# Performance work log

Hardware: AMD Instinct MI355X
Metric: run time of the kernel (lower is better)

## Reference

```python
import jax, jax.numpy as jnp
import numpy as np

B_J0 = 0.01
BETA = 1.8
GAMMA = 0.5
LENS = 0.5
HIGHT = 0.15
SCALE = 6.0
H1, H2, D_IN, D_OUT = 256, 256, 700, 20
BATCH, T = 128, 250


def spike_fn(x):
    # forward of ActFun_adp: Heaviside
    return (x > 0).astype(x.dtype)


def mem_update_adp(inputs, mem, spike, tau_adp, b, tau_m):
    alpha = jnp.exp(-1.0 / tau_m)
    ro = jnp.exp(-1.0 / tau_adp)
    b = ro * b + (1.0 - ro) * spike
    B = B_J0 + BETA * b
    mem = mem * alpha + (1.0 - alpha) * inputs - B * spike
    spike = spike_fn(mem - B)
    return mem, spike, b


def setup_inputs() -> dict:
    key = jax.random.key(0)
    ks = jax.random.split(key, 16)
    inp = {
        "x": jax.random.uniform(ks[0], (BATCH, T, D_IN), jnp.float32),
        "mem1_0": jax.random.uniform(ks[1], (BATCH, H1), jnp.float32),
        "mem2_0": jax.random.uniform(ks[2], (BATCH, H2), jnp.float32),
        "memo_0": jax.random.uniform(ks[3], (BATCH, D_OUT), jnp.float32),
        "Wi1": jax.random.normal(ks[4], (H1, D_IN), jnp.float32) * 0.05,
        "bi1": jnp.zeros((H1,), jnp.float32),
        "W11": jax.random.normal(ks[5], (H1, H1), jnp.float32) * 0.05,
        "b11": jnp.zeros((H1,), jnp.float32),
        "W12": jax.random.normal(ks[6], (H2, H1), jnp.float32) * 0.05,
        "b12": jnp.zeros((H2,), jnp.float32),
        "W22": jax.random.normal(ks[7], (H2, H2), jnp.float32) * 0.05,
        "b22": jnp.zeros((H2,), jnp.float32),
        "Wo": jax.random.normal(ks[8], (D_OUT, H2), jnp.float32) * 0.05,
        "bo": jnp.zeros((D_OUT,), jnp.float32),
        "tau_adp_h1": 150.0 + 10.0 * jax.random.normal(ks[9], (H1,), jnp.float32),
        "tau_adp_h2": 150.0 + 10.0 * jax.random.normal(ks[10], (H2,), jnp.float32),
        "tau_m_h1": 20.0 + 5.0 * jax.random.normal(ks[11], (H1,), jnp.float32),
        "tau_m_h2": 20.0 + 5.0 * jax.random.normal(ks[12], (H2,), jnp.float32),
        "tau_m_o": 20.0 + 5.0 * jax.random.normal(ks[13], (D_OUT,), jnp.float32),
    }
    return inp


def reference(x, mem1_0, mem2_0, memo_0, Wi1, bi1, W11, b11, W12, b12,
              W22, b22, Wo, bo, tau_adp_h1, tau_adp_h2, tau_m_h1, tau_m_h2, tau_m_o):
    B = x.shape[0]
    sp1_0 = jnp.zeros_like(mem1_0)
    sp2_0 = jnp.zeros_like(mem2_0)
    b1_0 = jnp.full_like(mem1_0, B_J0)
    b2_0 = jnp.full_like(mem2_0, B_J0)
    acc0 = jnp.zeros((B, Wo.shape[0]), x.dtype)
    alpha_o = jnp.exp(-1.0 / tau_m_o)

    def step(carry, inp):
        x_t, i = inp
        mem1, sp1, b1, mem2, sp2, b2, memo, acc = carry
        h1_in = x_t @ Wi1.T + bi1 + sp1 @ W11.T + b11
        mem1, sp1, b1 = mem_update_adp(h1_in, mem1, sp1, tau_adp_h1, b1, tau_m_h1)
        h2_in = sp1 @ W12.T + b12 + sp2 @ W22.T + b22
        mem2, sp2, b2 = mem_update_adp(h2_in, mem2, sp2, tau_adp_h2, b2, tau_m_h2)
        memo = memo * alpha_o + (1.0 - alpha_o) * (sp2 @ Wo.T + bo)
        acc = acc + jnp.where(i > 10, jax.nn.softmax(memo, axis=1), 0.0)
        return (mem1, sp1, b1, mem2, sp2, b2, memo, acc), None

    xs = jnp.swapaxes(x, 0, 1)  # [T, B, D_in]
    ts = jnp.arange(xs.shape[0])
    carry, _ = jax.lax.scan(step, (mem1_0, sp1_0, b1_0, mem2_0, sp2_0, b2_0, memo_0, acc0), (xs, ts))
    return carry[-1]  # accumulated softmax output [B, D_out]
```

## Files before the change

### kernel.cpp

```cpp
#include <hip/hip_runtime.h>
#include <math.h>

#define BATCH 128
#define T 250
#define D_IN 700
#define H 256
#define D_OUT 20

typedef float v2f __attribute__((ext_vector_type(2)));
typedef __attribute__((ext_vector_type(8))) short bf16x8;
typedef __attribute__((ext_vector_type(4))) float f32x4;
typedef __attribute__((ext_vector_type(4))) unsigned u32x4;

static __device__ __forceinline__ unsigned short f2b(float f) {
    unsigned u = __float_as_uint(f);
    u += 0x7FFFu + ((u >> 16) & 1u);
    return (unsigned short)(u >> 16);
}

static __device__ __forceinline__ void bar() {
    asm volatile("s_waitcnt lgkmcnt(0)" ::: "memory");
    __builtin_amdgcn_s_barrier();
    asm volatile("" ::: "memory");
}

#define PIDX(c) (10 * ((c) >> 3) + ((c) & 7))
#define QIDX(c) (6 * ((c) >> 2) + ((c) & 3))

#define N_C1 (257 * 512)
#define N_C2 (257 * 288)
#define N_WP (256 * 704)

__global__ void prep_k(const float* __restrict__ Wi1, const float* __restrict__ W11,
                       const float* __restrict__ W12, const float* __restrict__ W22,
                       const float* __restrict__ Wo,
                       unsigned short* __restrict__ Wi1p, unsigned short* __restrict__ C1,
                       unsigned short* __restrict__ C2) {
    int idx = blockIdx.x * 256 + threadIdx.x;
    if (idx < N_C1) {
        int k = idx >> 9, p = idx & 511;
        float v = 0.f;
        if (k < H) v = (p < 256) ? W12[p * H + k] : W11[(p - 256) * H + k];
        C1[idx] = f2b(v);
        return;
    }
    idx -= N_C1;
    if (idx < N_C2) {
        int k = idx / 288, p = idx - k * 288;
        float v = 0.f;
        if (k < H) {
            if (p < 256) v = W22[p * H + k];
            else if (p - 256 < D_OUT) v = Wo[(p - 256) * H + k];
        }
        C2[idx] = f2b(v);
        return;
    }
    idx -= N_C2;
    if (idx < N_WP) {
        int h = idx / 704, k = idx - h * 704;
        Wi1p[idx] = (k < D_IN) ? f2b(Wi1[h * D_IN + k]) : (unsigned short)0;
    }
}

__global__ __launch_bounds__(256) void gemm_u_k(const float* __restrict__ x,
                                                const unsigned short* __restrict__ Wi1p,
                                                const float* __restrict__ bi1,
                                                float* __restrict__ U) {
    const int lane = threadIdx.x & 63;
    const int wv = threadIdx.x >> 6;
    const int quad = lane >> 4;
    const int nl = lane & 15;
    const int mbase = blockIdx.x * 64 + wv * 16;
    const int m = mbase + nl;

    f32x4 acc[16];
#pragma unroll
    for (int i = 0; i < 16; ++i) acc[i] = (f32x4)(0.f);

    float bias[16];
#pragma unroll
    for (int nt = 0; nt < 16; ++nt) bias[nt] = bi1[nt * 16 + nl];

    const float* xrow = x + (size_t)m * D_IN;
    const unsigned short* brow = Wi1p + nl * 704 + quad * 8;

    for (int k0 = 0; k0 < 704; k0 += 32) {
        int ka = k0 + quad * 8;
        int ka2 = (ka + 4 <= 696) ? ka + 4 : 696;
        float4 q0 = *(const float4*)(xrow + ka);
        float4 q1 = *(const float4*)(xrow + ka2);
        bf16x8 af;
        af[0] = (short)f2b(q0.x); af[1] = (short)f2b(q0.y);
        af[2] = (short)f2b(q0.z); af[3] = (short)f2b(q0.w);
        af[4] = (short)f2b(q1.x); af[5] = (short)f2b(q1.y);
        af[6] = (short)f2b(q1.z); af[7] = (short)f2b(q1.w);

        const unsigned short* bp = brow + k0;
        bf16x8 bf[16];
#pragma unroll
        for (int nt = 0; nt < 16; ++nt)
            bf[nt] = *(const bf16x8*)(bp + nt * 16 * 704);
#pragma unroll
        for (int nt = 0; nt < 16; ++nt)
            acc[nt] = __builtin_amdgcn_mfma_f32_16x16x32_bf16(af, bf[nt], acc[nt], 0, 0, 0);
    }

#pragma unroll
    for (int nt = 0; nt < 16; ++nt) {
#pragma unroll
        for (int r = 0; r < 4; ++r) {
            U[(size_t)(mbase + quad * 4 + r) * H + nt * 16 + nl] = acc[nt][r] + bias[nt];
        }
    }
}

static __device__ __forceinline__ void ld8b(const unsigned* __restrict__ L, int c,
                                            const unsigned short* __restrict__ Cb,
                                            unsigned l8, u32x4* b) {
    uint4 ia = *(const uint4*)(L + c);
    uint4 ib = *(const uint4*)(L + c + 4);
    unsigned I[8] = {ia.x, ia.y, ia.z, ia.w, ib.x, ib.y, ib.z, ib.w};
#pragma unroll
    for (int jj = 0; jj < 8; ++jj)
        b[jj] = *(const u32x4*)(Cb + ((unsigned)I[jj] << 9) + l8);
}

static __device__ __forceinline__ void acc8b(const u32x4* b, v2f* a) {
#pragma unroll
    for (int jj = 0; jj < 8; ++jj) {
#pragma unroll
        for (int q = 0; q < 4; ++q) {
            unsigned u = b[jj][q];
            v2f t;
            t.x = __uint_as_float(u << 16);
            t.y = __uint_as_float(u & 0xffff0000u);
            a[q] += t;
        }
    }
}

static __device__ __forceinline__ void gatherB(const unsigned* __restrict__ L, int n,
                                               const unsigned short* __restrict__ Cb,
                                               unsigned l8, v2f* a) {
    a[0] = (v2f)(0.f); a[1] = (v2f)(0.f); a[2] = (v2f)(0.f); a[3] = (v2f)(0.f);
    int nr = (n + 7) & ~7;
    if (nr == 0) return;
    u32x4 x[8], y[8];
    ld8b(L, 0, Cb, l8, x);
    if (nr == 8) { acc8b(x, a); return; }
    ld8b(L, 8, Cb, l8, y);
    int c = 16;
    for (; c + 16 <= nr; c += 16) {
        acc8b(x, a); ld8b(L, c, Cb, l8, x);
        acc8b(y, a); ld8b(L, c + 8, Cb, l8, y);
    }
    if (nr - c == 8) {
        acc8b(x, a); ld8b(L, c, Cb, l8, x);
        acc8b(y, a); acc8b(x, a);
    } else {
        acc8b(x, a); acc8b(y, a);
    }
}

static __device__ __forceinline__ void ld8c(const unsigned* __restrict__ L, int c,
                                            const unsigned short* Cb,
                                            unsigned mo, unsigned ao,
                                            uint2* m, unsigned* av) {
    uint4 ia = *(const uint4*)(L + c);
    uint4 ib = *(const uint4*)(L + c + 4);
    unsigned I[8] = {ia.x, ia.y, ia.z, ia.w, ib.x, ib.y, ib.z, ib.w};
#pragma unroll
    for (int jj = 0; jj < 8; ++jj) {
        const unsigned short* p = Cb + (unsigned)I[jj] * 288u;
        m[jj] = *(const uint2*)(p + mo);
        av[jj] = *(const unsigned*)(p + ao);
    }
}

static __device__ __forceinline__ void acc8c(const uint2* m, const unsigned* av,
                                             v2f* g, v2f& aA) {
#pragma unroll
    for (int jj = 0; jj < 8; ++jj) {
        unsigned u0 = m[jj].x, u1 = m[jj].y, uA = av[jj];
        v2f t0, t1, tA;
        t0.x = __uint_as_float(u0 << 16); t0.y = __uint_as_float(u0 & 0xffff0000u);
        t1.x = __uint_as_float(u1 << 16); t1.y = __uint_as_float(u1 & 0xffff0000u);
        tA.x = __uint_as_float(uA << 16); tA.y = __uint_as_float(uA & 0xffff0000u);
        g[0] += t0; g[1] += t1; aA += tA;
    }
}

static __device__ __forceinline__ void gather2(const unsigned* __restrict__ L, int n,
                                               const unsigned short* Cb,
                                               unsigned mo, unsigned ao,
                                               v2f* g, v2f& aA) {
    g[0] = (v2f)(0.f); g[1] = (v2f)(0.f); aA = (v2f)(0.f);
    int nr = (n + 7) & ~7;
    if (nr == 0) return;
    uint2 xm[8], ym[8]; unsigned xa[8], ya[8];
    ld8c(L, 0, Cb, mo, ao, xm, xa);
    if (nr == 8) { acc8c(xm, xa, g, aA); return; }
    ld8c(L, 8, Cb, mo, ao, ym, ya);
    int c = 16;
    for (; c + 16 <= nr; c += 16) {
        acc8c(xm, xa, g, aA); ld8c(L, c, Cb, mo, ao, xm, xa);
        acc8c(ym, ya, g, aA); ld8c(L, c + 8, Cb, mo, ao, ym, ya);
    }
    if (nr - c == 8) {
        acc8c(xm, xa, g, aA); ld8c(L, c, Cb, mo, ao, xm, xa);
        acc8c(ym, ya, g, aA); acc8c(xm, xa, g, aA);
    } else {
        acc8c(xm, xa, g, aA); acc8c(ym, ya, g, aA);
    }
}

__global__ __launch_bounds__(512, 1) void recurrent_k(
    const float* __restrict__ U,
    const float* __restrict__ mem1_0, const float* __restrict__ mem2_0,
    const float* __restrict__ memo_0,
    const float* __restrict__ b11v, const float* __restrict__ b12v,
    const float* __restrict__ b22v, const float* __restrict__ bov,
    const float* __restrict__ tau_adp_h1, const float* __restrict__ tau_adp_h2,
    const float* __restrict__ tau_m_h1, const float* __restrict__ tau_m_h2,
    const float* __restrict__ tau_m_o,
    const unsigned short* __restrict__ C1b, const unsigned short* __restrict__ C2b,
    float* __restrict__ out)
{
    const int tid = threadIdx.x;
    const int lane = tid & 63;
    const int w = tid >> 6;
    const bool trackA = (w < 4);
    const int wt = w & 3;
    const int bi = blockIdx.x;
    const int j = wt * 64 + lane;
    const unsigned l8 = (unsigned)lane * 8;
    const unsigned mo = (unsigned)lane * 4;
    const unsigned ao = 256u + 2u * (unsigned)(lane & 15);

    __shared__ float PA[4][2][640];
    __shared__ float PB[4][2][432];
    __shared__ __align__(16) unsigned short C2L[193 * 288];
    __shared__ __align__(16) unsigned lists[8][128];

    {
        unsigned* dst = (unsigned*)C2L;
        const unsigned* src = (const unsigned*)C2b;
        for (int i = tid; i < 193 * 144; i += 512)
            dst[i] = (i < 192 * 144) ? src[i] : 0u;
    }
    for (int i = tid; i < 4 * 2 * 640; i += 512) ((float*)PA)[i] = 0.f;
    for (int i = tid; i < 4 * 2 * 432; i += 512) ((float*)PB)[i] = 0.f;

    float mem1 = 0.f, b1 = 0.01f, spk1 = 0.f;
    float al1 = 0.f, ro1 = 0.f, oma1 = 0.f, omr1 = 0.f, b11p = 0.f;
    if (trackA) {
        mem1 = mem1_0[bi * H + j];
        al1 = __expf(-1.f / tau_m_h1[j]);
        ro1 = __expf(-1.f / tau_adp_h1[j]);
        oma1 = 1.f - al1; omr1 = 1.f - ro1;
        b11p = b11v[j];
    }

    float mem2 = 0.f, b2 = 0.01f, spk2 = 0.f;
    float al2 = 0.f, ro2 = 0.f, oma2 = 0.f, omr2 = 0.f, bs2 = 0.f;
    if (!trackA) {
        mem2 = mem2_0[bi * H + j];
        al2 = __expf(-1.f / tau_m_h2[j]);
        ro2 = __expf(-1.f / tau_adp_h2[j]);
        oma2 = 1.f - al2; omr2 = 1.f - ro2;
        bs2 = b12v[j] + b22v[j];
    }

    float memo = 0.f, alo = 0.f, omo = 0.f, bop = 0.f, acco = 0.f;
    const bool outl = (w == 4 && lane < D_OUT);
    if (outl) {
        memo = memo_0[bi * D_OUT + lane];
        alo = __expf(-1.f / tau_m_o[lane]);
        omo = 1.f - alo;
        bop = bov[lane];
    }

    const float* Up = U + (size_t)bi * T * H + j;
    float u_cur = trackA ? *Up : 0.f;
    float u_nxt = 0.f;
    const unsigned long long below = (1ull << lane) - 1ull;

    const int pidx_self = 320 + PIDX(j);
    const int pidx_j = PIDX(j);
    const int qidx_j = QIDX(j);
    const int qidx_out = 384 + 6 * (lane >> 2) + (lane & 3);

    __syncthreads();

    for (int t = 0; t < 252; ++t) {
        const int rbA = (t + 1) & 1;
        const int wbA = t & 1;
        const int rsB = (t + 1) & 1;
        const int wsB = t & 1;

        if (trackA && t < 250) {
            float g11 = PA[0][rbA][pidx_self] + PA[1][rbA][pidx_self] +
                        PA[2][rbA][pidx_self] + PA[3][rbA][pidx_self];
            float h1 = u_cur + b11p + g11;
            b1 = ro1 * b1 + omr1 * spk1;
            float B1 = 0.01f + 1.8f * b1;
            mem1 = mem1 * al1 + oma1 * h1 - B1 * spk1;
            spk1 = (mem1 - B1 > 0.f) ? 1.f : 0.f;

            unsigned long long m = __ballot(spk1 != 0.f);
            int n = __popcll(m);
            unsigned* L = lists[w];
            if (spk1 != 0.f) L[__popcll(m & below)] = (unsigned)j;
            L[n + lane] = 256u;
            asm volatile("s_waitcnt lgkmcnt(0)" ::: "memory");
            __builtin_amdgcn_wave_barrier();

            u_nxt = Up[H];
            Up += H;

            v2f a[4];
            gatherB(L, n, C1b, l8, a);

            float* pw = &PA[wt][wbA][10 * lane];
            *(v2f*)(pw + 0) = a[0];
            *(v2f*)(pw + 2) = a[1];
            *(v2f*)(pw + 4) = a[2];
            *(v2f*)(pw + 6) = a[3];
            u_cur = u_nxt;
        }

        if (w == 4 && t >= 2) {
            float e = 0.f;
            if (lane < D_OUT) {
                float aO = PB[0][rsB][qidx_out] + PB[1][rsB][qidx_out] +
                           PB[2][rsB][qidx_out] + PB[3][rsB][qidx_out];
                memo = memo * alo + omo * (bop + aO);
                e = __expf(memo);
            }
            if (t >= 13) {
                float s = e;
#pragma unroll
                for (int dd = 16; dd >= 1; dd >>= 1) s += __shfl_xor(s, dd, 32);
                if (lane < D_OUT) acco += __fdividef(e, s);
            }
        }

        if (!trackA && t >= 1 && t < 251) {
            float g12 = PA[0][rbA][pidx_j] + PA[1][rbA][pidx_j] +
                        PA[2][rbA][pidx_j] + PA[3][rbA][pidx_j];
            float g22 = PB[0][rsB][qidx_j] + PB[1][rsB][qidx_j] +
                        PB[2][rsB][qidx_j] + PB[3][rsB][qidx_j];
            float h2 = bs2 + g22 + g12;
            b2 = ro2 * b2 + omr2 * spk2;
            float B2 = 0.01f + 1.8f * b2;
            mem2 = mem2 * al2 + oma2 * h2 - B2 * spk2;
            spk2 = (mem2 - B2 > 0.f) ? 1.f : 0.f;

            unsigned long long m = __ballot(spk2 != 0.f);
            int n = __popcll(m);
            unsigned* L = lists[w];
            if (spk2 != 0.f) L[__popcll(m & below)] = (unsigned)j;
            L[n + lane] = (wt == 3) ? 256u : 192u;
            asm volatile("s_waitcnt lgkmcnt(0)" ::: "memory");
            __builtin_amdgcn_wave_barrier();

            v2f g[2]; v2f aA;
            if (wt == 3) {
                gather2(L, n, C2b, mo, ao, g, aA);
            } else {
                gather2(L, n, (const unsigned short*)C2L, mo, ao, g, aA);
            }

            float* pw = &PB[wt][wsB][6 * lane];
            *(v2f*)(pw + 0) = g[0];
            *(v2f*)(pw + 2) = g[1];
            if (lane < 16) {
                float* pa = &PB[wt][wsB][384 + 6 * (lane >> 1) + 2 * (lane & 1)];
                *(v2f*)pa = aA;
            }
        }

        bar();
    }

    if (outl) out[bi * D_OUT + lane] = acco;
}

extern "C" void kernel_launch(void* const* d_in, const int* in_sizes, int n_in,
                              void* d_out, int out_size, void* d_ws, size_t ws_size,
                              hipStream_t stream) {
    const float* x          = (const float*)d_in[0];
    const float* mem1_0     = (const float*)d_in[1];
    const float* mem2_0     = (const float*)d_in[2];
    const float* memo_0     = (const float*)d_in[3];
    const float* Wi1        = (const float*)d_in[4];
    const float* bi1        = (const float*)d_in[5];
    const float* W11        = (const float*)d_in[6];
    const float* b11        = (const float*)d_in[7];
    const float* W12        = (const float*)d_in[8];
    const float* b12        = (const float*)d_in[9];
    const float* W22        = (const float*)d_in[10];
    const float* b22        = (const float*)d_in[11];
    const float* Wo         = (const float*)d_in[12];
    const float* bo         = (const float*)d_in[13];
    const float* tau_adp_h1 = (const float*)d_in[14];
    const float* tau_adp_h2 = (const float*)d_in[15];
    const float* tau_m_h1   = (const float*)d_in[16];
    const float* tau_m_h2   = (const float*)d_in[17];
    const float* tau_m_o    = (const float*)d_in[18];

    float* U = (float*)d_ws;
    unsigned short* C1b  = (unsigned short*)(U + ((size_t)BATCH * T + 1) * H);
    unsigned short* C2b  = C1b + N_C1;
    unsigned short* Wi1p = C2b + N_C2;

    int prep_total = N_C1 + N_C2 + N_WP;
    prep_k<<<(prep_total + 255) / 256, 256, 0, stream>>>(
        Wi1, W11, W12, W22, Wo, Wi1p, C1b, C2b);

    gemm_u_k<<<(BATCH * T) / 64, 256, 0, stream>>>(x, Wi1p, bi1, U);

    recurrent_k<<<BATCH, 512, 0, stream>>>(U, mem1_0, mem2_0, memo_0,
                                           b11, b12, b22, bo,
                                           tau_adp_h1, tau_adp_h2,
                                           tau_m_h1, tau_m_h2, tau_m_o,
                                           C1b, C2b, (float*)d_out);
}
```

Before: 393.3 us.

## Split recurrent layers into paired producer/consumer blocks with global ring handoff

The single 512-thread block per batch row, which ran both layers in lockstep, is split into two 256-thread blocks. One runs layer 1 and publishes its layer-2 input contributions through a 16-slot global ring buffer with progress counters. The layer-2/output block spins on those counters, so the two layers run as a decoupled pipeline with backpressure instead of sharing a per-step barrier. The input projection U is also stored as bf16 to halve its traffic. The cost is spin-wait polling and a reliance on co-residency of paired blocks (256 blocks on the device) to avoid deadlock, plus some bf16 rounding of the input currents.

```diff
diff --git a/kernel.cpp b/kernel.cpp
--- a/kernel.cpp
+++ b/kernel.cpp
@@ -6,6 +6,7 @@
 #define D_IN 700
 #define H 256
 #define D_OUT 20
+#define RING 16
 
 typedef float v2f __attribute__((ext_vector_type(2)));
 typedef __attribute__((ext_vector_type(8))) short bf16x8;
@@ -16,12 +17,6 @@
     unsigned u = __float_as_uint(f);
     u += 0x7FFFu + ((u >> 16) & 1u);
     return (unsigned short)(u >> 16);
-}
-
-static __device__ __forceinline__ void bar() {
-    asm volatile("s_waitcnt lgkmcnt(0)" ::: "memory");
-    __builtin_amdgcn_s_barrier();
-    asm volatile("" ::: "memory");
 }
 
 #define PIDX(c) (10 * ((c) >> 3) + ((c) & 7))
@@ -65,7 +60,7 @@
 __global__ __launch_bounds__(256) void gemm_u_k(const float* __restrict__ x,
                                                 const unsigned short* __restrict__ Wi1p,
                                                 const float* __restrict__ bi1,
-                                                float* __restrict__ U) {
+                                                unsigned short* __restrict__ Ub) {
     const int lane = threadIdx.x & 63;
     const int wv = threadIdx.x >> 6;
     const int quad = lane >> 4;
@@ -109,7 +104,8 @@
     for (int nt = 0; nt < 16; ++nt) {
 #pragma unroll
         for (int r = 0; r < 4; ++r) {
-            U[(size_t)(mbase + quad * 4 + r) * H + nt * 16 + nl] = acc[nt][r] + bias[nt];
+            Ub[(size_t)(mbase + quad * 4 + r) * H + nt * 16 + nl] =
+                f2b(acc[nt][r] + bias[nt]);
         }
     }
 }
@@ -214,8 +210,8 @@
     }
 }
 
-__global__ __launch_bounds__(512, 1) void recurrent_k(
-    const float* __restrict__ U,
+__global__ __launch_bounds__(256, 1) void recurrent_k(
+    const unsigned short* __restrict__ Ub,
     const float* __restrict__ mem1_0, const float* __restrict__ mem2_0,
     const float* __restrict__ memo_0,
     const float* __restrict__ b11v, const float* __restrict__ b12v,
@@ -224,55 +220,122 @@
     const float* __restrict__ tau_m_h1, const float* __restrict__ tau_m_h2,
     const float* __restrict__ tau_m_o,
     const unsigned short* __restrict__ C1b, const unsigned short* __restrict__ C2b,
+    float* __restrict__ G12all, int* __restrict__ prog, int* __restrict__ bdone,
     float* __restrict__ out)
 {
     const int tid = threadIdx.x;
     const int lane = tid & 63;
-    const int w = tid >> 6;
-    const bool trackA = (w < 4);
-    const int wt = w & 3;
-    const int bi = blockIdx.x;
-    const int j = wt * 64 + lane;
-    const unsigned l8 = (unsigned)lane * 8;
-    const unsigned mo = (unsigned)lane * 4;
-    const unsigned ao = 256u + 2u * (unsigned)(lane & 15);
+    const int wt = tid >> 6;
+    const int bi = blockIdx.x >> 1;
+    const bool isA = (blockIdx.x & 1) == 0;
+    const int j = (wt << 6) + lane;
 
     __shared__ float PA[4][2][640];
     __shared__ float PB[4][2][432];
     __shared__ __align__(16) unsigned short C2L[193 * 288];
-    __shared__ __align__(16) unsigned lists[8][128];
+    __shared__ __align__(16) unsigned listsA[4][128];
+    __shared__ __align__(16) unsigned listsB[4][128];
+
+    float* G12 = G12all + (size_t)bi * RING * 256;
+    int* progp = prog + bi;
+    int* bdonep = bdone + bi;
+    const unsigned long long below = (1ull << lane) - 1ull;
+
+    if (isA) {
+        for (int i = tid; i < 4 * 2 * 640; i += 256) ((float*)PA)[i] = 0.f;
+
+        float mem1 = mem1_0[bi * H + j];
+        float al1 = __expf(-1.f / tau_m_h1[j]);
+        float ro1 = __expf(-1.f / tau_adp_h1[j]);
+        float oma1 = 1.f - al1, omr1 = 1.f - ro1;
+        float b11p = b11v[j];
+        float b1 = 0.01f, spk1 = 0.f;
+
+        const unsigned short* Upb = Ub + (size_t)bi * T * H + j;
+        unsigned short ucur = *Upb;
+        const int pidx_self = 320 + PIDX(j);
+        const int pub_pi = PIDX(j);
+        int bd_c = 0;
+        __syncthreads();
+
+        for (int t = 0; t <= 250; ++t) {
+            const int rbA = (t + 1) & 1, wbA = t & 1;
+
+            if (t >= 1) {
+                float v = PA[0][rbA][pub_pi] + PA[1][rbA][pub_pi] +
+                          PA[2][rbA][pub_pi] + PA[3][rbA][pub_pi];
+                __hip_atomic_store(&G12[((t - 1) & (RING - 1)) * 256 + j], v,
+                                   __ATOMIC_RELAXED, __HIP_MEMORY_SCOPE_AGENT);
+            }
+
+            if (t < 250) {
+                float g11 = PA[0][rbA][pidx_self] + PA[1][rbA][pidx_self] +
+                            PA[2][rbA][pidx_self] + PA[3][rbA][pidx_self];
+                float u = __uint_as_float((unsigned)ucur << 16);
+                float h1 = u + b11p + g11;
+                b1 = ro1 * b1 + omr1 * spk1;
+                float B1 = 0.01f + 1.8f * b1;
+                mem1 = mem1 * al1 + oma1 * h1 - B1 * spk1;
+                spk1 = (mem1 - B1 > 0.f) ? 1.f : 0.f;
+
+                unsigned long long m = __ballot(spk1 != 0.f);
+                int n = __popcll(m);
+                unsigned* L = listsA[wt];
+                if (spk1 != 0.f) L[__popcll(m & below)] = (unsigned)j;
+                L[n + lane] = 256u;
+                asm volatile("s_waitcnt lgkmcnt(0)" ::: "memory");
+                __builtin_amdgcn_wave_barrier();
+
+                unsigned short unxt = Upb[H];
+                Upb += H;
+
+                v2f a[4];
+                gatherB(L, n, C1b, (unsigned)lane * 8, a);
+
+                float* pw = &PA[wt][wbA][10 * lane];
+                *(v2f*)(pw + 0) = a[0];
+                *(v2f*)(pw + 2) = a[1];
+                *(v2f*)(pw + 4) = a[2];
+                *(v2f*)(pw + 6) = a[3];
+                ucur = unxt;
+            }
+
+            if ((t & 7) == 0 && t > bd_c + 13) {
+                while (true) {
+                    bd_c = __hip_atomic_load(bdonep, __ATOMIC_RELAXED,
+                                             __HIP_MEMORY_SCOPE_AGENT);
+                    if (t <= bd_c + 13) break;
+                    __builtin_amdgcn_s_sleep(8);
+                }
+            }
+
+            asm volatile("s_waitcnt vmcnt(0) lgkmcnt(0)" ::: "memory");
+            __builtin_amdgcn_s_barrier();
+            asm volatile("" ::: "memory");
+            if (t >= 1 && tid == 0)
+                __hip_atomic_store(progp, t, __ATOMIC_RELAXED,
+                                   __HIP_MEMORY_SCOPE_AGENT);
+        }
+        return;
+    }
 
     {
         unsigned* dst = (unsigned*)C2L;
         const unsigned* src = (const unsigned*)C2b;
-        for (int i = tid; i < 193 * 144; i += 512)
+        for (int i = tid; i < 193 * 144; i += 256)
             dst[i] = (i < 192 * 144) ? src[i] : 0u;
     }
-    for (int i = tid; i < 4 * 2 * 640; i += 512) ((float*)PA)[i] = 0.f;
-    for (int i = tid; i < 4 * 2 * 432; i += 512) ((float*)PB)[i] = 0.f;
-
-    float mem1 = 0.f, b1 = 0.01f, spk1 = 0.f;
-    float al1 = 0.f, ro1 = 0.f, oma1 = 0.f, omr1 = 0.f, b11p = 0.f;
-    if (trackA) {
-        mem1 = mem1_0[bi * H + j];
-        al1 = __expf(-1.f / tau_m_h1[j]);
-        ro1 = __expf(-1.f / tau_adp_h1[j]);
-        oma1 = 1.f - al1; omr1 = 1.f - ro1;
-        b11p = b11v[j];
-    }
-
-    float mem2 = 0.f, b2 = 0.01f, spk2 = 0.f;
-    float al2 = 0.f, ro2 = 0.f, oma2 = 0.f, omr2 = 0.f, bs2 = 0.f;
-    if (!trackA) {
-        mem2 = mem2_0[bi * H + j];
-        al2 = __expf(-1.f / tau_m_h2[j]);
-        ro2 = __expf(-1.f / tau_adp_h2[j]);
-        oma2 = 1.f - al2; omr2 = 1.f - ro2;
-        bs2 = b12v[j] + b22v[j];
-    }
+    for (int i = tid; i < 4 * 2 * 432; i += 256) ((float*)PB)[i] = 0.f;
+
+    float mem2 = mem2_0[bi * H + j];
+    float al2 = __expf(-1.f / tau_m_h2[j]);
+    float ro2 = __expf(-1.f / tau_adp_h2[j]);
+    float oma2 = 1.f - al2, omr2 = 1.f - ro2;
+    float bs2 = b12v[j] + b22v[j];
+    float b2 = 0.01f, spk2 = 0.f;
 
     float memo = 0.f, alo = 0.f, omo = 0.f, bop = 0.f, acco = 0.f;
-    const bool outl = (w == 4 && lane < D_OUT);
+    const bool outl = (wt == 0 && lane < D_OUT);
     if (outl) {
         memo = memo_0[bi * D_OUT + lane];
         alo = __expf(-1.f / tau_m_o[lane]);
@@ -280,56 +343,25 @@
         bop = bov[lane];
     }
 
-    const float* Up = U + (size_t)bi * T * H + j;
-    float u_cur = trackA ? *Up : 0.f;
-    float u_nxt = 0.f;
-    const unsigned long long below = (1ull << lane) - 1ull;
-
-    const int pidx_self = 320 + PIDX(j);
-    const int pidx_j = PIDX(j);
+    const unsigned mo = (unsigned)lane * 4;
+    const unsigned ao = 256u + 2u * (unsigned)(lane & 15);
     const int qidx_j = QIDX(j);
     const int qidx_out = 384 + 6 * (lane >> 2) + (lane & 3);
-
+    float g12c = 0.f, g12n = 0.f;
     __syncthreads();
 
-    for (int t = 0; t < 252; ++t) {
-        const int rbA = (t + 1) & 1;
-        const int wbA = t & 1;
-        const int rsB = (t + 1) & 1;
-        const int wsB = t & 1;
-
-        if (trackA && t < 250) {
-            float g11 = PA[0][rbA][pidx_self] + PA[1][rbA][pidx_self] +
-                        PA[2][rbA][pidx_self] + PA[3][rbA][pidx_self];
-            float h1 = u_cur + b11p + g11;
-            b1 = ro1 * b1 + omr1 * spk1;
-            float B1 = 0.01f + 1.8f * b1;
-            mem1 = mem1 * al1 + oma1 * h1 - B1 * spk1;
-            spk1 = (mem1 - B1 > 0.f) ? 1.f : 0.f;
-
-            unsigned long long m = __ballot(spk1 != 0.f);
-            int n = __popcll(m);
-            unsigned* L = lists[w];
-            if (spk1 != 0.f) L[__popcll(m & below)] = (unsigned)j;
-            L[n + lane] = 256u;
-            asm volatile("s_waitcnt lgkmcnt(0)" ::: "memory");
-            __builtin_amdgcn_wave_barrier();
-
-            u_nxt = Up[H];
-            Up += H;
-
-            v2f a[4];
-            gatherB(L, n, C1b, l8, a);
-
-            float* pw = &PA[wt][wbA][10 * lane];
-            *(v2f*)(pw + 0) = a[0];
-            *(v2f*)(pw + 2) = a[1];
-            *(v2f*)(pw + 4) = a[2];
-            *(v2f*)(pw + 6) = a[3];
-            u_cur = u_nxt;
-        }
-
-        if (w == 4 && t >= 2) {
+    for (int tau = 0; tau <= 253; ++tau) {
+        if (tau >= 2 && tau <= 251) {
+            const int want = tau - 1;
+            while (__hip_atomic_load(progp, __ATOMIC_RELAXED,
+                                     __HIP_MEMORY_SCOPE_AGENT) < want)
+                __builtin_amdgcn_s_sleep(2);
+            g12n = __hip_atomic_load(&G12[((tau - 2) & (RING - 1)) * 256 + j],
+                                     __ATOMIC_RELAXED, __HIP_MEMORY_SCOPE_AGENT);
+        }
+        const int rsB = (tau + 1) & 1, wsB = tau & 1;
+
+        if (wt == 0 && tau >= 4) {
             float e = 0.f;
             if (lane < D_OUT) {
                 float aO = PB[0][rsB][qidx_out] + PB[1][rsB][qidx_out] +
@@ -337,7 +369,7 @@
                 memo = memo * alo + omo * (bop + aO);
                 e = __expf(memo);
             }
-            if (t >= 13) {
+            if (tau >= 15) {
                 float s = e;
 #pragma unroll
                 for (int dd = 16; dd >= 1; dd >>= 1) s += __shfl_xor(s, dd, 32);
@@ -345,12 +377,10 @@
             }
         }
 
-        if (!trackA && t >= 1 && t < 251) {
-            float g12 = PA[0][rbA][pidx_j] + PA[1][rbA][pidx_j] +
-                        PA[2][rbA][pidx_j] + PA[3][rbA][pidx_j];
+        if (tau >= 3 && tau <= 252) {
             float g22 = PB[0][rsB][qidx_j] + PB[1][rsB][qidx_j] +
                         PB[2][rsB][qidx_j] + PB[3][rsB][qidx_j];
-            float h2 = bs2 + g22 + g12;
+            float h2 = bs2 + g22 + g12c;
             b2 = ro2 * b2 + omr2 * spk2;
             float B2 = 0.01f + 1.8f * b2;
             mem2 = mem2 * al2 + oma2 * h2 - B2 * spk2;
@@ -358,18 +388,15 @@
 
             unsigned long long m = __ballot(spk2 != 0.f);
             int n = __popcll(m);
-            unsigned* L = lists[w];
+            unsigned* L = listsB[wt];
             if (spk2 != 0.f) L[__popcll(m & below)] = (unsigned)j;
             L[n + lane] = (wt == 3) ? 256u : 192u;
             asm volatile("s_waitcnt lgkmcnt(0)" ::: "memory");
             __builtin_amdgcn_wave_barrier();
 
             v2f g[2]; v2f aA;
-            if (wt == 3) {
-                gather2(L, n, C2b, mo, ao, g, aA);
-            } else {
-                gather2(L, n, (const unsigned short*)C2L, mo, ao, g, aA);
-            }
+            if (wt == 3) gather2(L, n, C2b, mo, ao, g, aA);
+            else gather2(L, n, (const unsigned short*)C2L, mo, ao, g, aA);
 
             float* pw = &PB[wt][wsB][6 * lane];
             *(v2f*)(pw + 0) = g[0];
@@ -379,8 +406,15 @@
                 *(v2f*)pa = aA;
             }
         }
-
-        bar();
+        g12c = g12n;
+
+        if (wt == 0 && lane == 0)
+            __hip_atomic_store(bdonep, tau, __ATOMIC_RELAXED,
+                               __HIP_MEMORY_SCOPE_AGENT);
+
+        asm volatile("s_waitcnt lgkmcnt(0)" ::: "memory");
+        __builtin_amdgcn_s_barrier();
+        asm volatile("" ::: "memory");
     }
 
     if (outl) out[bi * D_OUT + lane] = acco;
@@ -409,20 +443,26 @@
     const float* tau_m_h2   = (const float*)d_in[17];
     const float* tau_m_o    = (const float*)d_in[18];
 
-    float* U = (float*)d_ws;
-    unsigned short* C1b  = (unsigned short*)(U + ((size_t)BATCH * T + 1) * H);
+    unsigned short* Ub   = (unsigned short*)d_ws;
+    unsigned short* C1b  = Ub + (size_t)(BATCH * T + 1) * H;
     unsigned short* C2b  = C1b + N_C1;
     unsigned short* Wi1p = C2b + N_C2;
+    float* G12           = (float*)(Wi1p + N_WP);
+    int* prog            = (int*)(G12 + (size_t)BATCH * RING * 256);
+    int* bdone           = prog + BATCH;
+
+    hipMemsetAsync(prog, 0, 2 * BATCH * sizeof(int), stream);
 
     int prep_total = N_C1 + N_C2 + N_WP;
     prep_k<<<(prep_total + 255) / 256, 256, 0, stream>>>(
         Wi1, W11, W12, W22, Wo, Wi1p, C1b, C2b);
 
-    gemm_u_k<<<(BATCH * T) / 64, 256, 0, stream>>>(x, Wi1p, bi1, U);
-
-    recurrent_k<<<BATCH, 512, 0, stream>>>(U, mem1_0, mem2_0, memo_0,
-                                           b11, b12, b22, bo,
-                                           tau_adp_h1, tau_adp_h2,
-                                           tau_m_h1, tau_m_h2, tau_m_o,
-                                           C1b, C2b, (float*)d_out);
-}
+    gemm_u_k<<<(BATCH * T) / 64, 256, 0, stream>>>(x, Wi1p, bi1, Ub);
+
+    recurrent_k<<<2 * BATCH, 256, 0, stream>>>(Ub, mem1_0, mem2_0, memo_0,
+                                               b11, b12, b22, bo,
+                                               tau_adp_h1, tau_adp_h2,
+                                               tau_m_h1, tau_m_h2, tau_m_o,
+                                               C1b, C2b, G12, prog, bdone,
+                                               (float*)d_out);
+}
```

Result: slower. 635.4 us (+61.5%).

## Store recurrent weights in fp32 and drop LDS-staged W22 copy

Applied to the files above, without the earlier changes.

Recurrent weight matrices C1/C2 are now kept in fp32 instead of bf16, so the spike-driven row gathers load floats directly and skip the bf16 unpack. The LDS copy of most of C2 and the per-wave choice between LDS and global sources are removed, and every wave gathers from global memory. This removes unpack ALU work and the LDS staging setup, but doubles the bytes fetched per gathered row and moves the W22 gathers from LDS to global/L2.

```diff
diff --git a/kernel.cpp b/kernel.cpp
--- a/kernel.cpp
+++ b/kernel.cpp
@@ -10,7 +10,6 @@
 typedef float v2f __attribute__((ext_vector_type(2)));
 typedef __attribute__((ext_vector_type(8))) short bf16x8;
 typedef __attribute__((ext_vector_type(4))) float f32x4;
-typedef __attribute__((ext_vector_type(4))) unsigned u32x4;
 
 static __device__ __forceinline__ unsigned short f2b(float f) {
     unsigned u = __float_as_uint(f);
@@ -34,14 +33,14 @@
 __global__ void prep_k(const float* __restrict__ Wi1, const float* __restrict__ W11,
                        const float* __restrict__ W12, const float* __restrict__ W22,
                        const float* __restrict__ Wo,
-                       unsigned short* __restrict__ Wi1p, unsigned short* __restrict__ C1,
-                       unsigned short* __restrict__ C2) {
+                       unsigned short* __restrict__ Wi1p, float* __restrict__ C1,
+                       float* __restrict__ C2) {
     int idx = blockIdx.x * 256 + threadIdx.x;
     if (idx < N_C1) {
         int k = idx >> 9, p = idx & 511;
         float v = 0.f;
         if (k < H) v = (p < 256) ? W12[p * H + k] : W11[(p - 256) * H + k];
-        C1[idx] = f2b(v);
+        C1[idx] = v;
         return;
     }
     idx -= N_C1;
@@ -52,7 +51,7 @@
             if (p < 256) v = W22[p * H + k];
             else if (p - 256 < D_OUT) v = Wo[(p - 256) * H + k];
         }
-        C2[idx] = f2b(v);
+        C2[idx] = v;
         return;
     }
     idx -= N_C2;
@@ -114,103 +113,93 @@
     }
 }
 
-static __device__ __forceinline__ void ld8b(const unsigned* __restrict__ L, int c,
-                                            const unsigned short* __restrict__ Cb,
-                                            unsigned l8, u32x4* b) {
+static __device__ __forceinline__ void ld8f(const unsigned* __restrict__ L, int c,
+                                            const float* __restrict__ Cb, unsigned l8,
+                                            f32x4* ba, f32x4* bb) {
     uint4 ia = *(const uint4*)(L + c);
     uint4 ib = *(const uint4*)(L + c + 4);
     unsigned I[8] = {ia.x, ia.y, ia.z, ia.w, ib.x, ib.y, ib.z, ib.w};
 #pragma unroll
-    for (int jj = 0; jj < 8; ++jj)
-        b[jj] = *(const u32x4*)(Cb + ((unsigned)I[jj] << 9) + l8);
-}
-
-static __device__ __forceinline__ void acc8b(const u32x4* b, v2f* a) {
-#pragma unroll
-    for (int jj = 0; jj < 8; ++jj) {
-#pragma unroll
-        for (int q = 0; q < 4; ++q) {
-            unsigned u = b[jj][q];
-            v2f t;
-            t.x = __uint_as_float(u << 16);
-            t.y = __uint_as_float(u & 0xffff0000u);
-            a[q] += t;
-        }
-    }
-}
-
-static __device__ __forceinline__ void gatherB(const unsigned* __restrict__ L, int n,
-                                               const unsigned short* __restrict__ Cb,
-                                               unsigned l8, v2f* a) {
-    a[0] = (v2f)(0.f); a[1] = (v2f)(0.f); a[2] = (v2f)(0.f); a[3] = (v2f)(0.f);
+    for (int j = 0; j < 8; ++j) {
+        const float* p = Cb + ((unsigned)I[j] << 9) + l8;
+        ba[j] = *(const f32x4*)p;
+        bb[j] = *(const f32x4*)(p + 4);
+    }
+}
+
+static __device__ __forceinline__ void acc8f(const f32x4* ba, const f32x4* bb,
+                                             f32x4& A0, f32x4& A1) {
+#pragma unroll
+    for (int j = 0; j < 8; ++j) { A0 += ba[j]; A1 += bb[j]; }
+}
+
+static __device__ __forceinline__ void gather8(const unsigned* __restrict__ L, int n,
+                                               const float* __restrict__ Cb, unsigned l8,
+                                               f32x4& A0, f32x4& A1) {
+    A0 = (f32x4)(0.f);
+    A1 = (f32x4)(0.f);
     int nr = (n + 7) & ~7;
     if (nr == 0) return;
-    u32x4 x[8], y[8];
-    ld8b(L, 0, Cb, l8, x);
-    if (nr == 8) { acc8b(x, a); return; }
-    ld8b(L, 8, Cb, l8, y);
+    f32x4 xa[8], xb[8], ya[8], yb[8];
+    ld8f(L, 0, Cb, l8, xa, xb);
+    if (nr == 8) { acc8f(xa, xb, A0, A1); return; }
+    ld8f(L, 8, Cb, l8, ya, yb);
     int c = 16;
     for (; c + 16 <= nr; c += 16) {
-        acc8b(x, a); ld8b(L, c, Cb, l8, x);
-        acc8b(y, a); ld8b(L, c + 8, Cb, l8, y);
+        acc8f(xa, xb, A0, A1); ld8f(L, c, Cb, l8, xa, xb);
+        acc8f(ya, yb, A0, A1); ld8f(L, c + 8, Cb, l8, ya, yb);
     }
     if (nr - c == 8) {
-        acc8b(x, a); ld8b(L, c, Cb, l8, x);
-        acc8b(y, a); acc8b(x, a);
+        acc8f(xa, xb, A0, A1); ld8f(L, c, Cb, l8, xa, xb);
+        acc8f(ya, yb, A0, A1); acc8f(xa, xb, A0, A1);
     } else {
-        acc8b(x, a); acc8b(y, a);
-    }
-}
-
-static __device__ __forceinline__ void ld8c(const unsigned* __restrict__ L, int c,
-                                            const unsigned short* Cb,
+        acc8f(xa, xb, A0, A1); acc8f(ya, yb, A0, A1);
+    }
+}
+
+static __device__ __forceinline__ void ld8d(const unsigned* __restrict__ L, int c,
+                                            const float* __restrict__ Cb,
                                             unsigned mo, unsigned ao,
-                                            uint2* m, unsigned* av) {
+                                            f32x4* m, v2f* av) {
     uint4 ia = *(const uint4*)(L + c);
     uint4 ib = *(const uint4*)(L + c + 4);
     unsigned I[8] = {ia.x, ia.y, ia.z, ia.w, ib.x, ib.y, ib.z, ib.w};
 #pragma unroll
-    for (int jj = 0; jj < 8; ++jj) {
-        const unsigned short* p = Cb + (unsigned)I[jj] * 288u;
-        m[jj] = *(const uint2*)(p + mo);
-        av[jj] = *(const unsigned*)(p + ao);
-    }
-}
-
-static __device__ __forceinline__ void acc8c(const uint2* m, const unsigned* av,
-                                             v2f* g, v2f& aA) {
-#pragma unroll
-    for (int jj = 0; jj < 8; ++jj) {
-        unsigned u0 = m[jj].x, u1 = m[jj].y, uA = av[jj];
-        v2f t0, t1, tA;
-        t0.x = __uint_as_float(u0 << 16); t0.y = __uint_as_float(u0 & 0xffff0000u);
-        t1.x = __uint_as_float(u1 << 16); t1.y = __uint_as_float(u1 & 0xffff0000u);
-        tA.x = __uint_as_float(uA << 16); tA.y = __uint_as_float(uA & 0xffff0000u);
-        g[0] += t0; g[1] += t1; aA += tA;
-    }
-}
-
-static __device__ __forceinline__ void gather2(const unsigned* __restrict__ L, int n,
-                                               const unsigned short* Cb,
-                                               unsigned mo, unsigned ao,
-                                               v2f* g, v2f& aA) {
-    g[0] = (v2f)(0.f); g[1] = (v2f)(0.f); aA = (v2f)(0.f);
+    for (int j = 0; j < 8; ++j) {
+        const float* p = Cb + (unsigned)I[j] * 288u;
+        m[j] = *(const f32x4*)(p + mo);
+        av[j] = *(const v2f*)(p + ao);
+    }
+}
+
+static __device__ __forceinline__ void acc8d(const f32x4* m, const v2f* av,
+                                             f32x4& G, v2f& aA) {
+#pragma unroll
+    for (int j = 0; j < 8; ++j) { G += m[j]; aA += av[j]; }
+}
+
+static __device__ __forceinline__ void gather2f(const unsigned* __restrict__ L, int n,
+                                                const float* __restrict__ Cb,
+                                                unsigned mo, unsigned ao,
+                                                f32x4& G, v2f& aA) {
+    G = (f32x4)(0.f);
+    aA = (v2f)(0.f);
     int nr = (n + 7) & ~7;
     if (nr == 0) return;
-    uint2 xm[8], ym[8]; unsigned xa[8], ya[8];
-    ld8c(L, 0, Cb, mo, ao, xm, xa);
-    if (nr == 8) { acc8c(xm, xa, g, aA); return; }
-    ld8c(L, 8, Cb, mo, ao, ym, ya);
+    f32x4 xm[8], ym[8]; v2f xa[8], ya[8];
+    ld8d(L, 0, Cb, mo, ao, xm, xa);
+    if (nr == 8) { acc8d(xm, xa, G, aA); return; }
+    ld8d(L, 8, Cb, mo, ao, ym, ya);
     int c = 16;
     for (; c + 16 <= nr; c += 16) {
-        acc8c(xm, xa, g, aA); ld8c(L, c, Cb, mo, ao, xm, xa);
-        acc8c(ym, ya, g, aA); ld8c(L, c + 8, Cb, mo, ao, ym, ya);
+        acc8d(xm, xa, G, aA); ld8d(L, c, Cb, mo, ao, xm, xa);
+        acc8d(ym, ya, G, aA); ld8d(L, c + 8, Cb, mo, ao, ym, ya);
     }
     if (nr - c == 8) {
-        acc8c(xm, xa, g, aA); ld8c(L, c, Cb, mo, ao, xm, xa);
-        acc8c(ym, ya, g, aA); acc8c(xm, xa, g, aA);
+        acc8d(xm, xa, G, aA); ld8d(L, c, Cb, mo, ao, xm, xa);
+        acc8d(ym, ya, G, aA); acc8d(xm, xa, G, aA);
     } else {
-        acc8c(xm, xa, g, aA); acc8c(ym, ya, g, aA);
+        acc8d(xm, xa, G, aA); acc8d(ym, ya, G, aA);
     }
 }
 
@@ -223,7 +212,7 @@
     const float* __restrict__ tau_adp_h1, const float* __restrict__ tau_adp_h2,
     const float* __restrict__ tau_m_h1, const float* __restrict__ tau_m_h2,
     const float* __restrict__ tau_m_o,
-    const unsigned short* __restrict__ C1b, const unsigned short* __restrict__ C2b,
+    const float* __restrict__ C1f, const float* __restrict__ C2f,
     float* __restrict__ out)
 {
     const int tid = threadIdx.x;
@@ -239,15 +228,8 @@
 
     __shared__ float PA[4][2][640];
     __shared__ float PB[4][2][432];
-    __shared__ __align__(16) unsigned short C2L[193 * 288];
     __shared__ __align__(16) unsigned lists[8][128];
 
-    {
-        unsigned* dst = (unsigned*)C2L;
-        const unsigned* src = (const unsigned*)C2b;
-        for (int i = tid; i < 193 * 144; i += 512)
-            dst[i] = (i < 192 * 144) ? src[i] : 0u;
-    }
     for (int i = tid; i < 4 * 2 * 640; i += 512) ((float*)PA)[i] = 0.f;
     for (int i = tid; i < 4 * 2 * 432; i += 512) ((float*)PB)[i] = 0.f;
 
@@ -318,14 +300,16 @@
             u_nxt = Up[H];
             Up += H;
 
-            v2f a[4];
-            gatherB(L, n, C1b, l8, a);
+            f32x4 A0, A1;
+            gather8(L, n, C1f, l8, A0, A1);
 
             float* pw = &PA[wt][wbA][10 * lane];
-            *(v2f*)(pw + 0) = a[0];
-            *(v2f*)(pw + 2) = a[1];
-            *(v2f*)(pw + 4) = a[2];
-            *(v2f*)(pw + 6) = a[3];
+            const v2f* ap = (const v2f*)&A0;
+            const v2f* bp = (const v2f*)&A1;
+            *(v2f*)(pw + 0) = ap[0];
+            *(v2f*)(pw + 2) = ap[1];
+            *(v2f*)(pw + 4) = bp[0];
+            *(v2f*)(pw + 6) = bp[1];
             u_cur = u_nxt;
         }
 
@@ -360,20 +344,17 @@
             int n = __popcll(m);
             unsigned* L = lists[w];
             if (spk2 != 0.f) L[__popcll(m & below)] = (unsigned)j;
-            L[n + lane] = (wt == 3) ? 256u : 192u;
+            L[n + lane] = 256u;
             asm volatile("s_waitcnt lgkmcnt(0)" ::: "memory");
             __builtin_amdgcn_wave_barrier();
 
-            v2f g[2]; v2f aA;
-            if (wt == 3) {
-                gather2(L, n, C2b, mo, ao, g, aA);
-            } else {
-                gather2(L, n, (const unsigned short*)C2L, mo, ao, g, aA);
-            }
+            f32x4 G; v2f aA;
+            gather2f(L, n, C2f, mo, ao, G, aA);
 
             float* pw = &PB[wt][wsB][6 * lane];
-            *(v2f*)(pw + 0) = g[0];
-            *(v2f*)(pw + 2) = g[1];
+            const v2f* gp = (const v2f*)&G;
+            *(v2f*)(pw + 0) = gp[0];
+            *(v2f*)(pw + 2) = gp[1];
             if (lane < 16) {
                 float* pa = &PB[wt][wsB][384 + 6 * (lane >> 1) + 2 * (lane & 1)];
                 *(v2f*)pa = aA;
@@ -410,13 +391,13 @@
     const float* tau_m_o    = (const float*)d_in[18];
 
     float* U = (float*)d_ws;
-    unsigned short* C1b  = (unsigned short*)(U + ((size_t)BATCH * T + 1) * H);
-    unsigned short* C2b  = C1b + N_C1;
-    unsigned short* Wi1p = C2b + N_C2;
+    float* C1f = U + ((size_t)BATCH * T + 1) * H;
+    float* C2f = C1f + N_C1;
+    unsigned short* Wi1p = (unsigned short*)(C2f + N_C2);
 
     int prep_total = N_C1 + N_C2 + N_WP;
     prep_k<<<(prep_total + 255) / 256, 256, 0, stream>>>(
-        Wi1, W11, W12, W22, Wo, Wi1p, C1b, C2b);
+        Wi1, W11, W12, W22, Wo, Wi1p, C1f, C2f);
 
     gemm_u_k<<<(BATCH * T) / 64, 256, 0, stream>>>(x, Wi1p, bi1, U);
 
@@ -424,5 +405,5 @@
                                            b11, b12, b22, bo,
                                            tau_adp_h1, tau_adp_h2,
                                            tau_m_h1, tau_m_h2, tau_m_o,
-                                           C1b, C2b, (float*)d_out);
-}
+                                           C1f, C2f, (float*)d_out);
+}
```

Result: slower. 611.0 us (+55.3%).
